# Optimization experiments

Hardware: AMD Instinct MI355X
Metric: run time of the kernel (lower is better)

Reference implementation:

```python
import jax, jax.numpy as jnp
import numpy as np
import math

F_DIM = 512
N_HEADS = 8
HEAD_DIM = F_DIM // N_HEADS
IMG = 16            # image_size
L = IMG ** 3        # voxel sequence length = 4096
PATCH = 196         # patch_number (ViT 14x14)
VIT_RES = 14
RES = 224           # VIEW_IMAGE_RES
SKETCH_DIM = 768
SIGMA = 1.5         # fixed kernel_size (torch draws randomly when None)
GN_GROUPS = 32


def position_encoding(d_model, length):
    pe = np.zeros((length, d_model), dtype=np.float32)
    position = np.arange(length, dtype=np.float32)[:, None]
    div_term = np.exp(np.arange(0, d_model, 2, dtype=np.float32) * -(math.log(10000.0) / d_model))
    pe[:, 0::2] = np.sin(position * div_term)
    pe[:, 1::2] = np.cos(position * div_term)
    return jnp.asarray(pe)


def get_voxel_coordinates(resolution, size=1.0):
    # centers of a resolution^3 grid spanning [-size/2, size/2]
    idx = np.arange(resolution, dtype=np.float32)
    g = np.stack(np.meshgrid(idx, idx, idx, indexing='ij'), -1).reshape(-1, 3)
    return (g + 0.5) / resolution * size - size / 2.0


VOXEL_PE = position_encoding(F_DIM, L)          # (L, F)
COND_PE = position_encoding(F_DIM, PATCH)       # (S, F)
VOXEL_PTS = jnp.asarray(get_voxel_coordinates(IMG))  # (L, 3)
_vg = np.arange(VIT_RES, dtype=np.float32)
VIT_PIXELS = jnp.asarray(np.stack(np.meshgrid(_vg, _vg, indexing='ij'), -1).reshape(PATCH, 2))  # (S, 2)


def setup_inputs() -> dict:
    key = jax.random.key(0)
    ks = jax.random.split(key, 12)
    B = 8
    s = 0.02
    return {
        'x': jax.random.normal(ks[0], (B, F_DIM, IMG, IMG, IMG), jnp.float32),
        'sketch_feature': jax.random.normal(ks[1], (B, PATCH, SKETCH_DIM), jnp.float32),
        'projection_matrix': jax.random.normal(ks[2], (B, 1, 3, 3), jnp.float32),
        'gn_scale': jnp.ones((F_DIM,), jnp.float32),
        'gn_bias': jnp.zeros((F_DIM,), jnp.float32),
        'conv_w': jax.random.normal(ks[3], (F_DIM, F_DIM, 3, 3, 3), jnp.float32) * s,
        'conv_b': jnp.zeros((F_DIM,), jnp.float32),
        'k_w': jax.random.normal(ks[4], (F_DIM, SKETCH_DIM), jnp.float32) * s,
        'k_b': jnp.zeros((F_DIM,), jnp.float32),
        'v_w': jax.random.normal(ks[5], (F_DIM, SKETCH_DIM), jnp.float32) * s,
        'v_b': jnp.zeros((F_DIM,), jnp.float32),
        'in_proj_w': jax.random.normal(ks[6], (3 * F_DIM, F_DIM), jnp.float32) * s,
        'in_proj_b': jnp.zeros((3 * F_DIM,), jnp.float32),
        'out_w': jax.random.normal(ks[7], (F_DIM, F_DIM), jnp.float32) * s,
        'out_b': jnp.zeros((F_DIM,), jnp.float32),
    }


def _group_norm(x, scale, bias, groups=GN_GROUPS, eps=1e-5):
    B, C = x.shape[0], x.shape[1]
    xr = x.reshape(B, groups, C // groups, -1)
    m = xr.mean(axis=(2, 3), keepdims=True)
    v = xr.var(axis=(2, 3), keepdims=True)
    xn = ((xr - m) / jnp.sqrt(v + eps)).reshape(x.shape)
    shp = (1, C) + (1,) * (x.ndim - 2)
    return xn * scale.reshape(shp) + bias.reshape(shp)


def _attn_mask(projection_matrix):
    # project voxel centers, clamp to pixel grid, threshold cdist to vit patch centers
    P = projection_matrix[:, 0]                                  # (B,3,3)
    pc = jnp.einsum('bij,nj->bni', P, VOXEL_PTS)                 # (B,L,3)
    pixels = pc[..., 0:2] / pc[..., 2:3]
    pixels = jnp.clip(jnp.round(pixels), 0.0, RES - 1.0)         # clamp_pixel
    x_idx = (2.0 * pixels[..., 1:2] + 1.0) / RES * VIT_RES / 2.0
    y_idx = (2.0 * (RES - 1.0 - pixels[..., 0:1]) + 1.0) / RES * VIT_RES / 2.0
    ps = jnp.concatenate([x_idx, y_idx], -1) - 0.5               # (B,L,2)
    dist = jnp.linalg.norm(ps[:, :, None, :] - VIT_PIXELS[None, None], axis=-1)  # (B,L,S)
    return jnp.abs(dist) > (SIGMA - 1e-6)                        # True = masked out


def _forward(x, sketch_feature, projection_matrix, gn_scale, gn_bias, conv_w, conv_b,
             k_w, k_b, v_w, v_b, in_proj_w, in_proj_b, out_w, out_b):
    B = x.shape[0]
    # q path: GroupNorm -> SiLU -> Conv3d(3, pad 1)
    h = jax.nn.silu(_group_norm(x, gn_scale, gn_bias))
    h = jax.lax.conv_general_dilated(h, conv_w, window_strides=(1, 1, 1),
                                     padding=[(1, 1)] * 3,
                                     dimension_numbers=('NCDHW', 'OIDHW', 'NCDHW'))
    h = h + conv_b.reshape(1, F_DIM, 1, 1, 1)
    q = h.reshape(B, F_DIM, L).transpose(0, 2, 1) + VOXEL_PE[None]        # (B,L,F)

    mask = _attn_mask(projection_matrix)                                   # (B,L,S)

    k = sketch_feature @ k_w.T + k_b + COND_PE[None]                       # (B,S,F)
    v = sketch_feature @ v_w.T + v_b + COND_PE[None]

    # nn.MultiheadAttention (eval: no dropout)
    wq, wk, wv = jnp.split(in_proj_w, 3, axis=0)
    bq, bk, bv = jnp.split(in_proj_b, 3, axis=0)
    qh = (q @ wq.T + bq).reshape(B, L, N_HEADS, HEAD_DIM).transpose(0, 2, 1, 3)
    kh = (k @ wk.T + bk).reshape(B, PATCH, N_HEADS, HEAD_DIM).transpose(0, 2, 1, 3)
    vh = (v @ wv.T + bv).reshape(B, PATCH, N_HEADS, HEAD_DIM).transpose(0, 2, 1, 3)

    scores = jnp.einsum('bhld,bhsd->bhls', qh, kh) / math.sqrt(HEAD_DIM)   # (B,H,L,S)
    scores = jnp.where(mask[:, None], -jnp.inf, scores)                    # mask shared over heads
    attn = jax.nn.softmax(scores, axis=-1)
    o = jnp.einsum('bhls,bhsd->bhld', attn, vh)
    o = o.transpose(0, 2, 1, 3).reshape(B, L, F_DIM)
    o = o @ out_w.T + out_b                                                # (B,L,F)
    return o.transpose(0, 2, 1).reshape(B, F_DIM, IMG, IMG, IMG)


def reference(x, sketch_feature, projection_matrix, gn_scale, gn_bias, conv_w, conv_b,
              k_w, k_b, v_w, v_b, in_proj_w, in_proj_b, out_w, out_b):
    return _forward(x, sketch_feature, projection_matrix, gn_scale, gn_bias, conv_w, conv_b,
                    k_w, k_b, v_w, v_b, in_proj_w, in_proj_b, out_w, out_b)
```

## Files before the change

kernel.cpp:

```cpp
#include <hip/hip_runtime.h>

#define DEV static __device__ __forceinline__

typedef unsigned short u16;
typedef unsigned int u32;
typedef unsigned long long u64;
typedef float f32x4 __attribute__((ext_vector_type(4)));
typedef short bfrag __attribute__((ext_vector_type(8)));

#define FD 512
#define LV 4096
#define PV 5832

DEV float b2f(u16 u){ union{ u32 i; float f; } x; x.i = ((u32)u)<<16; return x.f; }
DEV u16 f2b(float f){ union{ float f; u32 i; } x; x.f = f; u32 r = x.i; r += 0x7fffu + ((r>>16)&1u); return (u16)(r>>16); }

DEV void g2l(const void* g, void* s){
  __builtin_amdgcn_global_load_lds((const __attribute__((address_space(1))) void*)g,
                                   (__attribute__((address_space(3))) void*)s, 16, 0, 0);
}

static const size_t o_wt  = 0;
static const size_t o_wq  = 14155776;
static const size_t o_ow  = 14680064;
static const size_t o_vpe = 15204352;
static const size_t o_cpe = 23592960;
static const size_t o_gn  = 23994368;
static const size_t o_mask= 23996416;
static const size_t o_khb = 25044992;
static const size_t o_vhb = 26748928;
static const size_t o_hp  = 36841472;
static const size_t o_qb  = 84617216;
static const size_t o_qh  = 118171648;
static const size_t o_skb = o_qh;
static const size_t o_kwb = o_qh + 2555904;
static const size_t o_vwb = o_qh + 3342336;
static const size_t o_wkb = o_qh + 4128768;
static const size_t o_wvb = o_qh + 4653056;
static const size_t o_ktb = o_qh + 5177344;
static const size_t o_vtb = o_qh + 6881280;

__global__ __launch_bounds__(256) void prep_all(const float* __restrict__ convw,
    const float* __restrict__ ipw, const float* __restrict__ ow,
    const float* __restrict__ sketch, const float* __restrict__ kw, const float* __restrict__ vw,
    u16* __restrict__ wt, u16* __restrict__ Wq, u16* __restrict__ Ow, u16* __restrict__ Skb,
    u16* __restrict__ Kwb, u16* __restrict__ Vwb, u16* __restrict__ Wkb, u16* __restrict__ Wvb){
  int blk = blockIdx.x, t = threadIdx.x;
  if (blk < 1024){
    int idx = blk*256 + t;
    const float* src = convw + (size_t)idx*27;
    float v[27];
    #pragma unroll
    for (int k=0;k<27;k++) v[k] = src[k];
    #pragma unroll
    for (int k=0;k<27;k++) wt[(size_t)k*262144 + idx] = f2b(v[k]);
  } else if (blk < 2048){ int i=(blk-1024)*256+t;  Wq[i]  = f2b(ipw[i]); }
  else if (blk < 3072){   int i=(blk-2048)*256+t;  Ow[i]  = f2b(ow[i]); }
  else if (blk < 7776){   int i=(blk-3072)*256+t;  if (i<1204224) Skb[i] = f2b(sketch[i]); }
  else if (blk < 9312){   int i=(blk-7776)*256+t;  Kwb[i] = f2b(kw[i]); }
  else if (blk < 10848){  int i=(blk-9312)*256+t;  Vwb[i] = f2b(vw[i]); }
  else if (blk < 11872){  int i=(blk-10848)*256+t; Wkb[i] = f2b(ipw[262144+i]); }
  else {                  int i=(blk-11872)*256+t; Wvb[i] = f2b(ipw[524288+i]); }
}

__global__ __launch_bounds__(256) void geom_prep(float* __restrict__ vpe, float* __restrict__ cpe,
    const float* __restrict__ proj, u64* __restrict__ maskb){
  int blk = blockIdx.x, t = threadIdx.x;
  if (blk < 4292){
    float* pe = (blk < 4096) ? vpe : cpe;
    int l = (blk < 4096) ? blk : blk - 4096;
    const float fac = -0.017988946039015984f;
    float dt = expf((float)(2*t) * fac);
    float ang = (float)l * dt;
    pe[(size_t)l*FD + 2*t]     = sinf(ang);
    pe[(size_t)l*FD + 2*t + 1] = cosf(ang);
    return;
  }
  int idx = (blk-4292)*256 + t;
  int b = idx >> 12, v = idx & 4095;
  float P[9];
  #pragma unroll
  for (int j=0;j<9;j++) P[j] = proj[b*9 + j];
  int zi=v>>8, yi=(v>>4)&15, xi=v&15;
  float pt0 = ((float)zi + 0.5f)/16.0f - 0.5f;
  float pt1 = ((float)yi + 0.5f)/16.0f - 0.5f;
  float pt2 = ((float)xi + 0.5f)/16.0f - 0.5f;
  float pc0 = __fadd_rn(__fadd_rn(__fmul_rn(P[0],pt0), __fmul_rn(P[1],pt1)), __fmul_rn(P[2],pt2));
  float pc1 = __fadd_rn(__fadd_rn(__fmul_rn(P[3],pt0), __fmul_rn(P[4],pt1)), __fmul_rn(P[5],pt2));
  float pc2 = __fadd_rn(__fadd_rn(__fmul_rn(P[6],pt0), __fmul_rn(P[7],pt1)), __fmul_rn(P[8],pt2));
  float r0 = __fdiv_rn(pc0, pc2);
  float r1 = __fdiv_rn(pc1, pc2);
  float px0 = fminf(fmaxf(rintf(r0), 0.f), 223.f);
  float px1 = fminf(fmaxf(rintf(r1), 0.f), 223.f);
  float x_idx = __fmul_rn(__fdiv_rn(__fadd_rn(__fmul_rn(2.f,px1),1.f), 224.f), 14.f) * 0.5f;
  float y_idx = __fmul_rn(__fdiv_rn(__fadd_rn(__fmul_rn(2.f,__fadd_rn(223.f,-px0)),1.f), 224.f), 14.f) * 0.5f;
  float ps0 = __fadd_rn(x_idx, -0.5f);
  float ps1 = __fadd_rn(y_idx, -0.5f);
  const float TH = 1.4999990463256836f;
  u64 abits[4] = {0,0,0,0};
  #pragma unroll 1
  for (int s=0;s<196;s++){
    int si = s/14, sj = s - si*14;
    float d0 = __fadd_rn(ps0, -(float)si);
    float d1 = __fadd_rn(ps1, -(float)sj);
    float dist = sqrtf(__fadd_rn(__fmul_rn(d0,d0), __fmul_rn(d1,d1)));
    if (!(fabsf(dist) > TH)) abits[s>>6] |= (1ull << (s&63));
  }
  u64* out = maskb + (size_t)idx*4;
  out[0]=abits[0]; out[1]=abits[1]; out[2]=abits[2]; out[3]=abits[3];
}

__global__ __launch_bounds__(256) void gn_stats(const float* __restrict__ x, float* __restrict__ stats){
  int bg = blockIdx.x;
  const float* base = x + (size_t)bg*65536;
  float s=0.f, q=0.f;
  for (int i=threadIdx.x;i<65536;i+=256){ float v = base[i]; s+=v; q+=v*v; }
  #pragma unroll
  for (int off=32; off>0; off>>=1){ s += __shfl_xor(s,off); q += __shfl_xor(q,off); }
  __shared__ float red[8];
  int w = threadIdx.x>>6;
  if ((threadIdx.x&63)==0){ red[w*2]=s; red[w*2+1]=q; }
  __syncthreads();
  if (threadIdx.x==0){
    float S=red[0]+red[2]+red[4]+red[6];
    float Q=red[1]+red[3]+red[5]+red[7];
    float m = S*(1.f/65536.f);
    float var = Q*(1.f/65536.f) - m*m;
    stats[bg] = m;
    stats[256+bg] = rsqrtf(var + 1e-5f);
  }
}

__global__ __launch_bounds__(256) void gn_apply_b(const float* __restrict__ x,
    const float* __restrict__ stats, const float* __restrict__ sc, const float* __restrict__ bi,
    u16* __restrict__ hp){
  int zb = blockIdx.x, cb = blockIdx.y, b = blockIdx.z;
  const float* xb = x + (size_t)b*FD*LV;
  u16* hpb = hp + (size_t)b*PV*FD;
  int t = threadIdx.x;
  int y = t>>4, xx = t&15;
  size_t hrow = ((size_t)(zb+1)*324 + (size_t)(y+1)*18 + (xx+1))*FD;
  int v = zb*256 + t;
  #pragma unroll 4
  for (int cc=0; cc<64; ++cc){
    int c = cb*64 + cc;
    float val = xb[(size_t)c*LV + v];
    int g = c>>4;
    float m = stats[b*32+g];
    float r = stats[256 + b*32+g];
    float xn = (val - m)*r*sc[c] + bi[c];
    hpb[hrow + c] = f2b(xn / (1.f + expf(-xn)));
  }
}

__global__ __launch_bounds__(256,4) void conv_mfma(const u16* __restrict__ hp,
    const u16* __restrict__ wt, const float* __restrict__ cbias,
    const float* __restrict__ vpe, u16* __restrict__ qb){
  __shared__ __align__(16) u16 Al[8192];
  __shared__ __align__(16) u16 Wl[8192];
  int tid = threadIdx.x;
  int w = tid>>6, l = tid&63;
  int v0 = blockIdx.x*128, n0 = blockIdx.y*128, b = blockIdx.z;
  int swz = ((l&7) ^ ((l>>3)&7))*8;
  size_t abase[4], wbase[4];
  #pragma unroll
  for (int j=0;j<4;j++){
    int r = w*32 + j*8 + (l>>3);
    int v = v0 + r;
    int z = v>>8, yy=(v>>4)&15, xx=v&15;
    abase[j] = ((size_t)b*PV + (size_t)(z*324 + yy*18 + xx))*FD + swz;
    wbase[j] = (size_t)(n0 + r)*FD + swz;
  }
  f32x4 zero4 = {0.f,0.f,0.f,0.f};
  f32x4 acc[4][4];
  #pragma unroll
  for (int i=0;i<4;i++)
    #pragma unroll
    for (int j=0;j<4;j++) acc[i][j] = zero4;
  int wr = (w>>1)*64, wc = (w&1)*64;
  for (int kk=0; kk<216; ++kk){
    int off = kk>>3;
    int ks  = (kk&7)<<6;
    int dz = off/9; int rem = off - dz*9; int dy = rem/3; int dx = rem - dy*3;
    size_t adelta = (size_t)(dz*324 + dy*18 + dx)*FD + ks;
    size_t wdelta = (size_t)off*262144 + ks;
    #pragma unroll
    for (int j=0;j<4;j++){
      g2l(hp + abase[j] + adelta, Al + (w*32 + j*8)*64);
      g2l(wt + wbase[j] + wdelta, Wl + (w*32 + j*8)*64);
    }
    __syncthreads();
    #pragma unroll
    for (int ks2=0; ks2<2; ++ks2){
      bfrag af[4], wf[4];
      #pragma unroll
      for (int i=0;i<4;i++){
        int ra = wr + i*16 + (l&15);
        af[i] = *(const bfrag*)(Al + ra*64 + (((ks2<<2) + (l>>4)) ^ (l&7))*8);
        int rb = wc + i*16 + (l&15);
        wf[i] = *(const bfrag*)(Wl + rb*64 + (((ks2<<2) + (l>>4)) ^ (l&7))*8);
      }
      #pragma unroll
      for (int i=0;i<4;i++)
        #pragma unroll
        for (int j=0;j<4;j++)
          acc[i][j] = __builtin_amdgcn_mfma_f32_16x16x32_bf16(af[i], wf[j], acc[i][j], 0,0,0);
    }
    __syncthreads();
  }
  #pragma unroll
  for (int i=0;i<4;i++)
    #pragma unroll
    for (int j=0;j<4;j++)
      #pragma unroll
      for (int rg=0;rg<4;rg++){
        int row = wr + i*16 + ((l>>4)<<2) + rg;
        int col = wc + j*16 + (l&15);
        int v = v0 + row, n = n0 + col;
        float cv = acc[i][j][rg] + cbias[n] + vpe[(size_t)v*FD + n];
        qb[((size_t)b*LV + v)*FD + n] = f2b(cv);
      }
}

template<bool TRANS>
__global__ __launch_bounds__(256,4) void gemm_mfma(const u16* __restrict__ A, const u16* __restrict__ W,
    const float* __restrict__ bias, void* __restrict__ Cout){
  __shared__ __align__(16) u16 Al[8192];
  __shared__ __align__(16) u16 Wl[8192];
  int tid = threadIdx.x;
  int w = tid>>6, l = tid&63;
  int m0 = blockIdx.x*128, n0 = blockIdx.y*128, b = blockIdx.z;
  int swz = ((l&7) ^ ((l>>3)&7))*8;
  size_t abase[4], wbase[4];
  #pragma unroll
  for (int j=0;j<4;j++){
    int r = w*32 + j*8 + (l>>3);
    abase[j] = ((size_t)b*LV + m0 + r)*FD + swz;
    wbase[j] = (size_t)(n0 + r)*FD + swz;
  }
  f32x4 zero4 = {0.f,0.f,0.f,0.f};
  f32x4 acc[4][4];
  #pragma unroll
  for (int i=0;i<4;i++)
    #pragma unroll
    for (int j=0;j<4;j++) acc[i][j] = zero4;
  int wr = (w>>1)*64, wc = (w&1)*64;
  for (int kk=0; kk<8; ++kk){
    size_t kd = (size_t)kk*64;
    #pragma unroll
    for (int j=0;j<4;j++){
      g2l(A + abase[j] + kd, Al + (w*32 + j*8)*64);
      g2l(W + wbase[j] + kd, Wl + (w*32 + j*8)*64);
    }
    __syncthreads();
    #pragma unroll
    for (int ks2=0; ks2<2; ++ks2){
      bfrag af[4], wf[4];
      #pragma unroll
      for (int i=0;i<4;i++){
        int ra = wr + i*16 + (l&15);
        af[i] = *(const bfrag*)(Al + ra*64 + (((ks2<<2) + (l>>4)) ^ (l&7))*8);
        int rb = wc + i*16 + (l&15);
        wf[i] = *(const bfrag*)(Wl + rb*64 + (((ks2<<2) + (l>>4)) ^ (l&7))*8);
      }
      #pragma unroll
      for (int i=0;i<4;i++)
        #pragma unroll
        for (int j=0;j<4;j++)
          acc[i][j] = __builtin_amdgcn_mfma_f32_16x16x32_bf16(af[i], wf[j], acc[i][j], 0,0,0);
    }
    __syncthreads();
  }
  #pragma unroll
  for (int i=0;i<4;i++)
    #pragma unroll
    for (int j=0;j<4;j++){
      if constexpr (TRANS){
        int row = m0 + wr + i*16 + ((l>>4)<<2);
        int col = n0 + wc + j*16 + (l&15);
        float bv = bias[col];
        float4 val = { acc[i][j][0]+bv, acc[i][j][1]+bv, acc[i][j][2]+bv, acc[i][j][3]+bv };
        *(float4*)&(((float*)Cout)[((size_t)b*FD + col)*LV + row]) = val;
      } else {
        #pragma unroll
        for (int rg=0;rg<4;rg++){
          int row = m0 + wr + i*16 + ((l>>4)<<2) + rg;
          int col = n0 + wc + j*16 + (l&15);
          ((u16*)Cout)[((size_t)b*LV + row)*FD + col] = f2b(acc[i][j][rg] + bias[col]);
        }
      }
    }
}

template<bool ADDPE>
__global__ __launch_bounds__(256,2) void gemm_kv(const u16* __restrict__ A0, const u16* __restrict__ A1,
    const u16* __restrict__ W0, const u16* __restrict__ W1,
    const float* __restrict__ b0, const float* __restrict__ b1,
    const float* __restrict__ pe, u16* __restrict__ C0, u16* __restrict__ C1, int K){
  const u16* A = blockIdx.z ? A1 : A0;
  const u16* W = blockIdx.z ? W1 : W0;
  const float* bias = blockIdx.z ? b1 : b0;
  u16* Cout = blockIdx.z ? C1 : C0;
  __shared__ __align__(16) u16 Al[4096];
  __shared__ __align__(16) u16 Wl[4096];
  int tid = threadIdx.x;
  int w = tid>>6, l = tid&63;
  int m0 = blockIdx.x*128, n0 = blockIdx.y*128;
  int sw_src = (((l&3) ^ ((l>>3)&3)))*8;
  int sw_rd  = (((l>>4) ^ ((l>>1)&3)))*8;
  size_t abase[2], wbase[2];
  #pragma unroll
  for (int j=0;j<2;j++){
    int r = (w*2+j)*16 + (l>>2);
    abase[j] = (size_t)(m0 + r)*K + sw_src;
    wbase[j] = (size_t)(n0 + r)*K + sw_src;
  }
  f32x4 zero4 = {0.f,0.f,0.f,0.f};
  f32x4 acc[4][4];
  #pragma unroll
  for (int i=0;i<4;i++)
    #pragma unroll
    for (int j=0;j<4;j++) acc[i][j] = zero4;
  int wr = (w>>1)*64, wc = (w&1)*64;
  for (int k0=0; k0<K; k0+=32){
    #pragma unroll
    for (int j=0;j<2;j++){
      g2l(A + abase[j] + k0, Al + (w*2+j)*512);
      g2l(W + wbase[j] + k0, Wl + (w*2+j)*512);
    }
    __syncthreads();
    bfrag af[4], wf[4];
    #pragma unroll
    for (int i=0;i<4;i++){
      int r  = wr + i*16 + (l&15);
      af[i] = *(const bfrag*)(Al + r*32 + sw_rd);
      int cn = wc + i*16 + (l&15);
      wf[i] = *(const bfrag*)(Wl + cn*32 + sw_rd);
    }
    #pragma unroll
    for (int i=0;i<4;i++)
      #pragma unroll
      for (int j=0;j<4;j++)
        acc[i][j] = __builtin_amdgcn_mfma_f32_16x16x32_bf16(af[i], wf[j], acc[i][j], 0,0,0);
    __syncthreads();
  }
  #pragma unroll
  for (int i=0;i<4;i++)
    #pragma unroll
    for (int j=0;j<4;j++)
      #pragma unroll
      for (int rg=0;rg<4;rg++){
        int row = m0 + wr + i*16 + ((l>>4)<<2) + rg;
        int col = n0 + wc + j*16 + (l&15);
        float cv = acc[i][j][rg] + bias[col];
        if constexpr (ADDPE) cv += pe[(size_t)(row % 196)*FD + col];
        Cout[(size_t)row*FD + col] = f2b(cv);
      }
}

__global__ __launch_bounds__(256) void attn_lit(const u16* __restrict__ qh,
    const u16* __restrict__ khb, const u16* __restrict__ vhb,
    const u64* __restrict__ maskb, u16* __restrict__ obuf){
  int v = blockIdx.x*256 + threadIdx.x;
  int h = blockIdx.y, b = blockIdx.z;
  const u64* mrow = maskb + ((size_t)b*LV + v)*4;
  u64 abits[4] = {mrow[0], mrow[1], mrow[2], mrow[3]};

  float qr[64];
  {
    const uint4* qp = (const uint4*)(qh + ((size_t)b*LV + v)*FD + h*64);
    #pragma unroll
    for (int c=0;c<8;c++){
      uint4 u = qp[c];
      qr[c*8+0]=b2f((u16)(u.x&0xffffu)); qr[c*8+1]=b2f((u16)(u.x>>16));
      qr[c*8+2]=b2f((u16)(u.y&0xffffu)); qr[c*8+3]=b2f((u16)(u.y>>16));
      qr[c*8+4]=b2f((u16)(u.z&0xffffu)); qr[c*8+5]=b2f((u16)(u.z>>16));
      qr[c*8+6]=b2f((u16)(u.w&0xffffu)); qr[c*8+7]=b2f((u16)(u.w>>16));
    }
  }
  const u16* kb = khb + (size_t)(b*196)*FD + h*64;
  const u16* vb = vhb + (size_t)(b*196)*FD + h*64;
  float o[64];
  #pragma unroll
  for (int d=0;d<64;d++) o[d]=0.f;
  float ssum = 0.f;
  for (int s=0;s<196;s++){
    if (!((abits[s>>6] >> (s&63)) & 1ull)) continue;
    const uint4* kr = (const uint4*)(kb + (size_t)s*FD);
    float dot = 0.f;
    #pragma unroll
    for (int c=0;c<8;c++){
      uint4 u = kr[c];
      dot += qr[c*8+0]*b2f((u16)(u.x&0xffffu)) + qr[c*8+1]*b2f((u16)(u.x>>16))
           + qr[c*8+2]*b2f((u16)(u.y&0xffffu)) + qr[c*8+3]*b2f((u16)(u.y>>16))
           + qr[c*8+4]*b2f((u16)(u.z&0xffffu)) + qr[c*8+5]*b2f((u16)(u.z>>16))
           + qr[c*8+6]*b2f((u16)(u.w&0xffffu)) + qr[c*8+7]*b2f((u16)(u.w>>16));
    }
    float e = expf(dot*0.125f);
    ssum += e;
    const uint4* vr = (const uint4*)(vb + (size_t)s*FD);
    #pragma unroll
    for (int c=0;c<8;c++){
      uint4 u = vr[c];
      o[c*8+0] += e*b2f((u16)(u.x&0xffffu)); o[c*8+1] += e*b2f((u16)(u.x>>16));
      o[c*8+2] += e*b2f((u16)(u.y&0xffffu)); o[c*8+3] += e*b2f((u16)(u.y>>16));
      o[c*8+4] += e*b2f((u16)(u.z&0xffffu)); o[c*8+5] += e*b2f((u16)(u.z>>16));
      o[c*8+6] += e*b2f((u16)(u.w&0xffffu)); o[c*8+7] += e*b2f((u16)(u.w>>16));
    }
  }
  float inv = (ssum > 0.f) ? 1.f/ssum : 0.f;
  u32* op = (u32*)(obuf + ((size_t)b*LV + v)*FD + h*64);
  #pragma unroll
  for (int c=0;c<32;c++){
    u32 lo = f2b(o[c*2]*inv);
    u32 hi = f2b(o[c*2+1]*inv);
    op[c] = lo | (hi<<16);
  }
}

extern "C" void kernel_launch(void* const* d_in, const int* in_sizes, int n_in,
                              void* d_out, int out_size, void* d_ws, size_t ws_size,
                              hipStream_t stream) {
  (void)in_sizes; (void)n_in; (void)out_size; (void)ws_size;
  const float* x_in  = (const float*)d_in[0];
  const float* sketch= (const float*)d_in[1];
  const float* projm = (const float*)d_in[2];
  const float* gnsc  = (const float*)d_in[3];
  const float* gnbi  = (const float*)d_in[4];
  const float* convw = (const float*)d_in[5];
  const float* convb = (const float*)d_in[6];
  const float* kw_in = (const float*)d_in[7];
  const float* kb_in = (const float*)d_in[8];
  const float* vw_in = (const float*)d_in[9];
  const float* vb_in = (const float*)d_in[10];
  const float* ipw   = (const float*)d_in[11];
  const float* ipb   = (const float*)d_in[12];
  const float* ow_in = (const float*)d_in[13];
  const float* ob_in = (const float*)d_in[14];
  char* ws = (char*)d_ws;
  u16*   wt   = (u16*)(ws + o_wt);
  u16*   Wq   = (u16*)(ws + o_wq);
  u16*   Ow   = (u16*)(ws + o_ow);
  float* vpe  = (float*)(ws + o_vpe);
  float* cpe  = (float*)(ws + o_cpe);
  float* stats= (float*)(ws + o_gn);
  u64*   maskb= (u64*)(ws + o_mask);
  u16*   khb  = (u16*)(ws + o_khb);
  u16*   vhb  = (u16*)(ws + o_vhb);
  u16*   hp   = (u16*)(ws + o_hp);
  u16*   qb   = (u16*)(ws + o_qb);
  u16*   qhb  = (u16*)(ws + o_qh);
  u16*   Skb  = (u16*)(ws + o_skb);
  u16*   Kwb  = (u16*)(ws + o_kwb);
  u16*   Vwb  = (u16*)(ws + o_vwb);
  u16*   Wkb  = (u16*)(ws + o_wkb);
  u16*   Wvb  = (u16*)(ws + o_wvb);
  u16*   ktb  = (u16*)(ws + o_ktb);
  u16*   vtb  = (u16*)(ws + o_vtb);
  u16*   obuf = qb;

  hipMemsetAsync(hp, 0, 47775744, stream);
  hipMemsetAsync((char*)Skb + 2408448, 0, 147456, stream);
  prep_all<<<12896,256,0,stream>>>(convw, ipw, ow_in, sketch, kw_in, vw_in,
                                   wt, Wq, Ow, Skb, Kwb, Vwb, Wkb, Wvb);
  geom_prep<<<4420,256,0,stream>>>(vpe, cpe, projm, maskb);
  gn_stats<<<256,256,0,stream>>>(x_in, stats);
  gemm_kv<true ><<<dim3(13,4,2),256,0,stream>>>(Skb, Skb, Kwb, Vwb, kb_in, vb_in, cpe, ktb, vtb, 768);
  gemm_kv<false><<<dim3(13,4,2),256,0,stream>>>(ktb, vtb, Wkb, Wvb, ipb+512, ipb+1024, nullptr, khb, vhb, 512);

  gn_apply_b<<<dim3(16,8,8),256,0,stream>>>(x_in, stats, gnsc, gnbi, hp);
  conv_mfma<<<dim3(32,4,8),256,0,stream>>>(hp, wt, convb, vpe, qb);
  gemm_mfma<false><<<dim3(32,4,8),256,0,stream>>>(qb, Wq, ipb, qhb);
  attn_lit<<<dim3(16,8,8),256,0,stream>>>(qhb, khb, vhb, maskb, obuf);
  gemm_mfma<true ><<<dim3(32,4,8),256,0,stream>>>(obuf, Ow, ob_in, d_out);
}
```

Baseline: 782.1 us.

## Stage transposes through LDS and group attention threads by spatial cubes

New measurement: 737.4 us. 5.7% less time.

```diff
diff --git a/kernel.cpp b/kernel.cpp
--- a/kernel.cpp
+++ b/kernel.cpp
@@ -45,15 +45,16 @@
     const float* __restrict__ sketch, const float* __restrict__ kw, const float* __restrict__ vw,
     u16* __restrict__ wt, u16* __restrict__ Wq, u16* __restrict__ Ow, u16* __restrict__ Skb,
     u16* __restrict__ Kwb, u16* __restrict__ Vwb, u16* __restrict__ Wkb, u16* __restrict__ Wvb){
+  __shared__ float raw[6912];
   int blk = blockIdx.x, t = threadIdx.x;
   if (blk < 1024){
-    int idx = blk*256 + t;
-    const float* src = convw + (size_t)idx*27;
-    float v[27];
-    #pragma unroll
-    for (int k=0;k<27;k++) v[k] = src[k];
-    #pragma unroll
-    for (int k=0;k<27;k++) wt[(size_t)k*262144 + idx] = f2b(v[k]);
+    size_t base = (size_t)blk*6912;
+    #pragma unroll
+    for (int j=0;j<27;j++) raw[j*256 + t] = convw[base + j*256 + t];
+    __syncthreads();
+    int rowb = blk*256;
+    #pragma unroll
+    for (int k=0;k<27;k++) wt[(size_t)k*262144 + rowb + t] = f2b(raw[t*27 + k]);
   } else if (blk < 2048){ int i=(blk-1024)*256+t;  Wq[i]  = f2b(ipw[i]); }
   else if (blk < 3072){   int i=(blk-2048)*256+t;  Ow[i]  = f2b(ow[i]); }
   else if (blk < 7776){   int i=(blk-3072)*256+t;  if (i<1204224) Skb[i] = f2b(sketch[i]); }
@@ -106,7 +107,9 @@
     float dist = sqrtf(__fadd_rn(__fmul_rn(d0,d0), __fmul_rn(d1,d1)));
     if (!(fabsf(dist) > TH)) abits[s>>6] |= (1ull << (s&63));
   }
-  u64* out = maskb + (size_t)idx*4;
+  int cube = (zi>>2)*16 + (yi>>2)*4 + (xi>>2);
+  int cl = cube*64 + (zi&3)*16 + (yi&3)*4 + (xi&3);
+  u64* out = maskb + ((size_t)b*4096 + cl)*4;
   out[0]=abits[0]; out[1]=abits[1]; out[2]=abits[2]; out[3]=abits[3];
 }
 
@@ -131,25 +134,34 @@
   }
 }
 
-__global__ __launch_bounds__(256) void gn_apply_b(const float* __restrict__ x,
+__global__ __launch_bounds__(256) void gn_apply_t(const float* __restrict__ x,
     const float* __restrict__ stats, const float* __restrict__ sc, const float* __restrict__ bi,
     u16* __restrict__ hp){
-  int zb = blockIdx.x, cb = blockIdx.y, b = blockIdx.z;
+  __shared__ u16 tile[64][66];
+  int vb = blockIdx.x, cb = blockIdx.y, b = blockIdx.z;
+  int t = threadIdx.x, w = t>>6, l = t&63;
+  int v0 = vb*64, c0 = cb*64;
   const float* xb = x + (size_t)b*FD*LV;
-  u16* hpb = hp + (size_t)b*PV*FD;
-  int t = threadIdx.x;
-  int y = t>>4, xx = t&15;
-  size_t hrow = ((size_t)(zb+1)*324 + (size_t)(y+1)*18 + (xx+1))*FD;
-  int v = zb*256 + t;
-  #pragma unroll 4
-  for (int cc=0; cc<64; ++cc){
-    int c = cb*64 + cc;
-    float val = xb[(size_t)c*LV + v];
+  #pragma unroll
+  for (int p=0;p<16;p++){
+    int cc = p*4 + w;
+    int c = c0 + cc;
+    float val = xb[(size_t)c*LV + v0 + l];
     int g = c>>4;
     float m = stats[b*32+g];
     float r = stats[256 + b*32+g];
     float xn = (val - m)*r*sc[c] + bi[c];
-    hpb[hrow + c] = f2b(xn / (1.f + expf(-xn)));
+    tile[cc][l] = f2b(xn / (1.f + expf(-xn)));
+  }
+  __syncthreads();
+  u16* hpb = hp + (size_t)b*PV*FD;
+  #pragma unroll
+  for (int p=0;p<16;p++){
+    int vv = p*4 + w;
+    int v = v0 + vv;
+    int z = v>>8, y = (v>>4)&15, xx = v&15;
+    size_t hrow = ((size_t)(z+1)*324 + (size_t)(y+1)*18 + (xx+1))*FD;
+    hpb[hrow + c0 + l] = tile[l][vv];
   }
 }
 
@@ -361,9 +373,14 @@
 __global__ __launch_bounds__(256) void attn_lit(const u16* __restrict__ qh,
     const u16* __restrict__ khb, const u16* __restrict__ vhb,
     const u64* __restrict__ maskb, u16* __restrict__ obuf){
-  int v = blockIdx.x*256 + threadIdx.x;
+  __shared__ u16 ot[4][64][66];
+  int t = threadIdx.x, w = t>>6, l = t&63;
   int h = blockIdx.y, b = blockIdx.z;
-  const u64* mrow = maskb + ((size_t)b*LV + v)*4;
+  int cube = blockIdx.x*4 + w;
+  int cz = cube>>4, cy = (cube>>2)&3, cx = cube&3;
+  int v = (cz*4 + (l>>4))*256 + (cy*4 + ((l>>2)&3))*16 + (cx*4 + (l&3));
+  int cl = cube*64 + l;
+  const u64* mrow = maskb + ((size_t)b*LV + cl)*4;
   u64 abits[4] = {mrow[0], mrow[1], mrow[2], mrow[3]};
 
   float qr[64];
@@ -409,12 +426,17 @@
     }
   }
   float inv = (ssum > 0.f) ? 1.f/ssum : 0.f;
-  u32* op = (u32*)(obuf + ((size_t)b*LV + v)*FD + h*64);
+  u32* orow = (u32*)&ot[w][l][0];
   #pragma unroll
   for (int c=0;c<32;c++){
     u32 lo = f2b(o[c*2]*inv);
     u32 hi = f2b(o[c*2+1]*inv);
-    op[c] = lo | (hi<<16);
+    orow[c] = lo | (hi<<16);
+  }
+  #pragma unroll 4
+  for (int s=0;s<64;s++){
+    int vs = (cz*4 + (s>>4))*256 + (cy*4 + ((s>>2)&3))*16 + (cx*4 + (s&3));
+    obuf[((size_t)b*LV + vs)*FD + h*64 + l] = ot[w][s][l];
   }
 }
 
@@ -468,7 +490,7 @@
   gemm_kv<true ><<<dim3(13,4,2),256,0,stream>>>(Skb, Skb, Kwb, Vwb, kb_in, vb_in, cpe, ktb, vtb, 768);
   gemm_kv<false><<<dim3(13,4,2),256,0,stream>>>(ktb, vtb, Wkb, Wvb, ipb+512, ipb+1024, nullptr, khb, vhb, 512);
 
-  gn_apply_b<<<dim3(16,8,8),256,0,stream>>>(x_in, stats, gnsc, gnbi, hp);
+  gn_apply_t<<<dim3(64,8,8),256,0,stream>>>(x_in, stats, gnsc, gnbi, hp);
   conv_mfma<<<dim3(32,4,8),256,0,stream>>>(hp, wt, convb, vpe, qb);
   gemm_mfma<false><<<dim3(32,4,8),256,0,stream>>>(qb, Wq, ipb, qhb);
   attn_lit<<<dim3(16,8,8),256,0,stream>>>(qhb, khb, vhb, maskb, obuf);
```
